# Performance work log

Hardware: AMD Instinct MI355X
Metric: run time of the kernel (lower is better)

The kernel has to match this reference:

```python
import jax, jax.numpy as jnp
import numpy as np

B, D, H, W, C = 2, 8, 56, 56, 128
NH = 4
HD = C // NH
WS = (7, 7)
HIDDEN = 4 * C
EPS = 1e-5


def layernorm(x, g, b):
    mu = jnp.mean(x, axis=-1, keepdims=True)
    var = jnp.var(x, axis=-1, keepdims=True)
    return (x - mu) * jax.lax.rsqrt(var + EPS) * g + b


def rearrange3d(x, gh, gw):
    b, d, h, w, c = x.shape
    x = x.reshape(b, d, h // gh, gh, w, c).swapaxes(2, 3).reshape(b, d, h, w, c)
    x = x.reshape(b, d, h, w // gw, gw, c).swapaxes(3, 4).reshape(b, d, h, w, c)
    return x


def restore3d(x, gh, gw):
    b, d, h, w, c = x.shape
    x = x.reshape(b, d, h, gw, w // gw, c).swapaxes(3, 4).reshape(b, d, h, w, c)
    x = x.reshape(b, d, gh, h // gh, w, c).swapaxes(2, 3).reshape(b, d, h, w, c)
    return x


def setup_inputs() -> dict:
    key = jax.random.key(0)
    ks = jax.random.split(key, 10)
    s = 0.02
    return {
        "x": jax.random.normal(ks[0], (B, D, H, W, C), jnp.float32),
        "norm1_g": jnp.ones((C,), jnp.float32),
        "norm1_b": jnp.zeros((C,), jnp.float32),
        "qkv_w": jax.random.normal(ks[1], (3 * C, C), jnp.float32) * s,
        "qkv_b": jnp.zeros((3 * C,), jnp.float32),
        "proj_w": jax.random.normal(ks[2], (C, C), jnp.float32) * s,
        "proj_b": jnp.zeros((C,), jnp.float32),
        "dw_w": jax.random.normal(ks[3], (3, 3, 1, C), jnp.float32) * s,  # HWIO depthwise
        "dw_b": jnp.zeros((C,), jnp.float32),
        "norm2_g": jnp.ones((C,), jnp.float32),
        "norm2_b": jnp.zeros((C,), jnp.float32),
        "fc1_w": jax.random.normal(ks[4], (HIDDEN, C), jnp.float32) * s,
        "fc1_b": jnp.zeros((HIDDEN,), jnp.float32),
        "fc2_w": jax.random.normal(ks[5], (C, HIDDEN), jnp.float32) * s,
        "fc2_b": jnp.zeros((C,), jnp.float32),
    }


def reference(x, norm1_g, norm1_b, qkv_w, qkv_b, proj_w, proj_b, dw_w, dw_b,
              norm2_g, norm2_b, fc1_w, fc1_b, fc2_w, fc2_b):
    b, d, h, w, c = x.shape
    gh, gw = h // WS[0], w // WS[1]  # 8, 8 (H,W divisible by window size -> no pad)
    shortcut = x

    # ---- part1: norm1 -> dwconv branch + windowed attention ----
    xn = layernorm(x, norm1_g, norm1_b)

    # depthwise 3x3 conv on each frame (B*D, H, W, C), SAME padding
    xc = jax.lax.conv_general_dilated(
        xn.reshape(b * d, h, w, c), dw_w, (1, 1), 'SAME',
        dimension_numbers=('NHWC', 'HWIO', 'NHWC'), feature_group_count=c)
    x_conv3d = (xc + dw_b).reshape(b, d, h, w, c)

    # interleaved regrouping, then window partition: (B*nW, N=D*7*7, C)
    xr = rearrange3d(xn, gh, gw)
    xw = xr.reshape(b, d, gh, WS[0], gw, WS[1], c)
    xw = xw.transpose(0, 2, 4, 1, 3, 5, 6).reshape(-1, d * WS[0] * WS[1], c)
    B_, N, _ = xw.shape

    # attention
    qkv = jnp.einsum('bnc,oc->bno', xw, qkv_w) + qkv_b
    qkv = qkv.reshape(B_, N, 3, NH, HD).transpose(2, 0, 3, 1, 4)  # (3, B_, nh, N, hd)
    q, k, v = qkv[0], qkv[1], qkv[2]
    scale = HD ** -0.5
    attn = jnp.einsum('bhnd,bhmd->bhnm', q * scale, k)
    attn = jax.nn.softmax(attn, axis=-1)
    out = jnp.einsum('bhnm,bhmd->bhnd', attn, v)
    out = out.transpose(0, 2, 1, 3).reshape(B_, N, c)
    out = jnp.einsum('bnc,oc->bno', out, proj_w) + proj_b

    # window reverse + restore grouping
    xo = out.reshape(b, gh, gw, d, WS[0], WS[1], c)
    xo = xo.transpose(0, 3, 1, 4, 2, 5, 6).reshape(b, d, h, w, c)
    xo = restore3d(xo, gh, gw)
    xo = xo + x_conv3d

    # ---- residuals + MLP ----
    x1 = shortcut + xo
    xm = layernorm(x1, norm2_g, norm2_b)
    xm = jnp.einsum('bdhwc,oc->bdhwo', xm, fc1_w) + fc1_b
    xm = jax.nn.gelu(xm, approximate=False)
    xm = jnp.einsum('bdhwo,co->bdhwc', xm, fc2_w) + fc2_b
    return x1 + xm


if __name__ == '__main__':
    inp = setup_inputs()
    y = reference(**inp)
    print(y.shape, y.dtype)
```

## Files before the change

kernel.cpp:

```cpp
#include <hip/hip_runtime.h>
#include <hip/hip_bf16.h>

#define NB 2
#define ND 8
#define NHH 56
#define NWW 56
#define NC 128
#define NHEAD 4
#define DHEAD 32
#define NSEQ 392
#define NWIN 128
#define NTOK (NB*ND*NHH*NWW)
#define NHID 512
#define EPSV 1e-5f
#define PIECE 12544

typedef unsigned int uint32;
typedef __attribute__((ext_vector_type(8))) short bf16x8;
typedef __attribute__((ext_vector_type(4))) float f32x4;
typedef __attribute__((ext_vector_type(16))) float f32x16;

__device__ __forceinline__ short f2bf(float x) {
  __hip_bfloat16 h = __float2bfloat16(x);
  return *reinterpret_cast<short*>(&h);
}
__device__ __forceinline__ float bflo(uint32 u) { return __uint_as_float(u << 16); }
__device__ __forceinline__ float bfhi(uint32 u) { return __uint_as_float(u & 0xffff0000u); }
__device__ __forceinline__ float fexp2(float x) {
  float e; asm("v_exp_f32 %0, %1" : "=v"(e) : "v"(x)); return e;
}

__device__ __forceinline__ int win_to_src(int grow) {
  int win = grow / NSEQ, n = grow % NSEQ;
  int b = win >> 6, gh = (win >> 3) & 7, gw = win & 7;
  int d = n / 49, rem = n % 49;
  int p = rem / 7, q = rem % 7;
  int h = p * 8 + gh, w = q * 8 + gw;
  return ((b * ND + d) * NHH + h) * NWW + w;
}

#define GLDS(gp, lp) \
  __builtin_amdgcn_global_load_lds( \
      (const __attribute__((address_space(1))) void*)(gp), \
      (__attribute__((address_space(3))) void*)(lp), 16, 0, 0)

__global__ void k_convw(const float* __restrict__ qkvw, const float* __restrict__ projw,
                        const float* __restrict__ fc1w, const float* __restrict__ fc2w,
                        short* __restrict__ out) {
  int i = blockIdx.x * 256 + threadIdx.x;
  float v; int n, k, K, base;
  if (i < 49152)       { v = qkvw[i];          n = i >> 7;          k = i & 127;   K = 128; base = 0; }
  else if (i < 65536)  { int l = i - 49152;  v = projw[l]; n = l >> 7; k = l & 127; K = 128; base = 49152; }
  else if (i < 131072) { int l = i - 65536;  v = fc1w[l];  n = l >> 7; k = l & 127; K = 128; base = 65536; }
  else                 { int l = i - 131072; v = fc2w[l];  n = l >> 9; k = l & 511; K = 512; base = 131072; }
  int k2 = (((k >> 3) ^ (n & 7)) << 3) | (k & 7);
  out[base + n * K + k2] = f2bf(v);
}

__global__ __launch_bounds__(256) void k_ln1(const float* __restrict__ xin,
    const float* __restrict__ g, const float* __restrict__ bsh, short* __restrict__ out) {
  int w = threadIdx.x >> 6, lane = threadIdx.x & 63;
  float g0 = g[2 * lane], g1 = g[2 * lane + 1];
  float b0 = bsh[2 * lane], b1 = bsh[2 * lane + 1];
  for (int r = blockIdx.x * 4 + w; r < NTOK; r += gridDim.x * 4) {
    int src = win_to_src(r);
    float2 v = *(const float2*)(xin + (long)src * NC + lane * 2);
    float s = v.x + v.y, s2 = v.x * v.x + v.y * v.y;
    #pragma unroll
    for (int m = 1; m < 64; m <<= 1) { s += __shfl_xor(s, m); s2 += __shfl_xor(s2, m); }
    float mu = s * (1.f / NC);
    float var = s2 * (1.f / NC) - mu * mu;
    float rr = rsqrtf(var + EPSV);
    uint32 p0 = (unsigned short)f2bf((v.x - mu) * rr * g0 + b0);
    uint32 p1 = (unsigned short)f2bf((v.y - mu) * rr * g1 + b1);
    int pos = (((lane >> 2) ^ (r & 7)) << 4) + ((lane & 3) << 2);
    *(uint32*)((char*)out + (long)r * 256 + pos) = p0 | (p1 << 16);
  }
}

__global__ void k_dwconv(const short* __restrict__ xn, const float* __restrict__ xorig,
                         const float* __restrict__ wgt, const float* __restrict__ bias,
                         short* __restrict__ out) {
  int idx = blockIdx.x * 256 + threadIdx.x;
  int cp = idx & 63;
  int wr = idx >> 6;
  int win = wr / NSEQ, n = wr % NSEQ;
  int b = win >> 6, gh = (win >> 3) & 7, gw = win & 7;
  int d = n / 49, rem = n % 49;
  int p = rem / 7, q = rem % 7;
  int h = p * 8 + gh, w = q * 8 + gw;
  int bd = b * ND + d;
  float a0 = bias[2 * cp], a1 = bias[2 * cp + 1];
  #pragma unroll
  for (int kh = 0; kh < 3; kh++) {
    int hh = h + kh - 1;
    if (hh < 0 || hh >= NHH) continue;
    #pragma unroll
    for (int kw = 0; kw < 3; kw++) {
      int ww = w + kw - 1;
      if (ww < 0 || ww >= NWW) continue;
      int wr2 = ((b << 6) + ((hh & 7) << 3) + (ww & 7)) * NSEQ
              + d * 49 + (hh >> 3) * 7 + (ww >> 3);
      int bo = (((cp >> 2) ^ (wr2 & 7)) << 4) + ((cp & 3) << 2);
      uint32 u = *(const uint32*)((const char*)xn + (long)wr2 * 256 + bo);
      a0 += bflo(u) * wgt[(kh * 3 + kw) * NC + 2 * cp];
      a1 += bfhi(u) * wgt[(kh * 3 + kw) * NC + 2 * cp + 1];
    }
  }
  int src = (bd * NHH + h) * NWW + w;
  float2 xo = *(const float2*)(xorig + ((long)src << 7) + 2 * cp);
  uint32 pk = (uint32)(unsigned short)f2bf(a0 + xo.x)
            | ((uint32)(unsigned short)f2bf(a1 + xo.y) << 16);
  *(uint32*)(out + ((long)wr << 7) + 2 * cp) = pk;
}

template <int BM, int NDIM, int KDIM, int MODE>
__global__ __launch_bounds__(256) void k_gemm_mfma(
    const short* __restrict__ A, const short* __restrict__ Wb,
    const float* __restrict__ bias, const short* __restrict__ xsum16,
    const float* __restrict__ g2, const float* __restrict__ b2,
    short* __restrict__ h0, short* __restrict__ h1,
    short* __restrict__ h2p, short* __restrict__ h3,
    void* __restrict__ O0, void* __restrict__ O1, void* __restrict__ O2) {
  constexpr int ABYTES = BM * 128;
  constexpr int MI = BM / 32;
  __shared__ char S[ABYTES + 16384];
  __shared__ int asrc[BM];
  int tid = threadIdx.x;
  int m0 = blockIdx.x * BM;
  int n0 = blockIdx.y * 128;
  int lane = tid & 63, w = tid >> 6;
  int wm = w & 1, wn = w >> 1;
  int c16 = lane & 15, g = lane >> 4;

  if constexpr (MODE == 3) {
    if (tid < BM) asrc[tid] = win_to_src(m0 + tid);
  }
  const short* Abase = A;
  int arow0 = m0;
  if constexpr (MODE == 3) {
    int pc = m0 / PIECE;
    Abase = (pc == 0) ? h0 : (pc == 1) ? h1 : (pc == 2) ? h2p : h3;
    arow0 = m0 - pc * PIECE;
  }

  f32x4 acc[MI][4];
  #pragma unroll
  for (int i = 0; i < MI; i++)
    #pragma unroll
    for (int j = 0; j < 4; j++) acc[i][j] = f32x4{0.f, 0.f, 0.f, 0.f};

  const int KSTEPS = KDIM / 64;
  for (int ks = 0; ks < KSTEPS; ks++) {
    int k0 = ks * 64;
    if (ks > 0) __syncthreads();
    #pragma unroll
    for (int i = 0; i < BM / 32; i++) {
      int idx = tid + i * 256;
      int row = idx >> 3, colq = idx & 7;
      GLDS(Abase + (long)(arow0 + row) * KDIM + k0 + colq * 8, S + (idx << 4));
    }
    #pragma unroll
    for (int i = 0; i < 4; i++) {
      int idx = tid + i * 256;
      int row = idx >> 3, colq = idx & 7;
      GLDS(Wb + (long)(n0 + row) * KDIM + k0 + colq * 8, S + ABYTES + (idx << 4));
    }
    asm volatile("s_waitcnt vmcnt(0)" ::: "memory");
    __syncthreads();
    #pragma unroll
    for (int kk = 0; kk < 2; kk++) {
      bf16x8 af[MI], bfr[4];
      #pragma unroll
      for (int i = 0; i < MI; i++) {
        int ra = wm * (BM / 2) + i * 16 + c16;
        int ba = (ra << 7) + ((g + kk * 4) << 4); ba ^= ((ra & 7) << 4);
        af[i] = *(const bf16x8*)(S + ba);
      }
      #pragma unroll
      for (int j = 0; j < 4; j++) {
        int rb = wn * 64 + j * 16 + c16;
        int bb = (rb << 7) + ((g + kk * 4) << 4); bb ^= ((rb & 7) << 4);
        bfr[j] = *(const bf16x8*)(S + ABYTES + bb);
      }
      #pragma unroll
      for (int i = 0; i < MI; i++)
        #pragma unroll
        for (int j = 0; j < 4; j++)
          acc[i][j] = __builtin_amdgcn_mfma_f32_16x16x32_bf16(af[i], bfr[j], acc[i][j], 0, 0, 0);
    }
  }
  __syncthreads();

  if constexpr (MODE == 0 || MODE == 1 || MODE == 2) {
    short* X1 = (short*)S;
    float qscale = (MODE == 0 && n0 == 0) ? 0.2550348658f : 1.0f;
    #pragma unroll
    for (int i = 0; i < MI; i++) {
      #pragma unroll
      for (int r = 0; r < 4; r++) {
        int row = wm * (BM / 2) + i * 16 + g * 4 + r;
        int sw7 = row & 7;
        #pragma unroll
        for (int j = 0; j < 4; j++) {
          int nl = wn * 64 + j * 16 + c16;
          float v = acc[i][j][r] + bias[n0 + nl];
          if constexpr (MODE == 2) {
            float u = v * (0.7978845608f + 0.035677408f * v * v);
            u = fmaxf(u, -15.f);
            float t = fexp2(u * -2.885390082f);
            v = 0.5f * v * (1.f + (1.f - t) / (1.f + t));
          } else {
            v *= qscale;
          }
          int ch = nl >> 3;
          int pos = (ch & 8) | ((ch & 7) ^ sw7);
          X1[(row << 7) + (pos << 3) + (nl & 7)] = f2bf(v);
        }
      }
    }
    __syncthreads();
    int cc = tid & 15;
    #pragma unroll
    for (int it8 = 0; it8 < BM / 16; it8++) {
      int row = it8 * 16 + (tid >> 4);
      int sw7 = row & 7;
      int pos = (cc & 8) | ((cc & 7) ^ sw7);
      uint4 val = *(const uint4*)(X1 + (row << 7) + (pos << 3));
      if constexpr (MODE == 0) {
        int m = m0 + row;
        int win = m / NSEQ, tok = m - win * NSEQ;
        short* OUT = (short*)((n0 == 0) ? O0 : (n0 == 128) ? O1 : O2);
        int head = cc >> 2, dim0 = (cc & 3) << 3;
        *(uint4*)(OUT + ((((long)(win * NHEAD + head)) * NSEQ + tok) << 5) + dim0) = val;
      } else if constexpr (MODE == 2) {
        int pco = m0 / PIECE;
        short* hpO = (pco == 0) ? h0 : (pco == 1) ? h1 : (pco == 2) ? h2p : h3;
        int mloc = m0 - pco * PIECE + row;
        *(uint4*)(hpO + ((long)mloc << 9) + n0 + (pos << 3)) = val;
      } else {
        long m = m0 + row;
        uint4 xs = *(const uint4*)(xsum16 + (m << 7) + (cc << 3));
        unsigned short* tv = (unsigned short*)&val;
        unsigned short* us = (unsigned short*)&xs;
        float xv[8];
        float s = 0.f, s2 = 0.f;
        #pragma unroll
        for (int e = 0; e < 8; e++) {
          xv[e] = bflo((uint32)tv[e]) + bflo((uint32)us[e]);
          s += xv[e]; s2 += xv[e] * xv[e];
        }
        #pragma unroll
        for (int mm = 1; mm < 16; mm <<= 1) { s += __shfl_xor(s, mm); s2 += __shfl_xor(s2, mm); }
        float mu = s * (1.f / NC);
        float var = s2 * (1.f / NC) - mu * mu;
        float rr2 = rsqrtf(var + EPSV);
        float4 gv0 = *(const float4*)(g2 + cc * 8);
        float4 gv1 = *(const float4*)(g2 + cc * 8 + 4);
        float4 bv0 = *(const float4*)(b2 + cc * 8);
        float4 bv1 = *(const float4*)(b2 + cc * 8 + 4);
        float gg[8] = {gv0.x, gv0.y, gv0.z, gv0.w, gv1.x, gv1.y, gv1.z, gv1.w};
        float bb[8] = {bv0.x, bv0.y, bv0.z, bv0.w, bv1.x, bv1.y, bv1.z, bv1.w};
        short xo[8], lo[8];
        #pragma unroll
        for (int e = 0; e < 8; e++) {
          xo[e] = f2bf(xv[e]);
          lo[e] = f2bf((xv[e] - mu) * rr2 * gg[e] + bb[e]);
        }
        *(uint4*)((short*)O0 + (m << 7) + (pos << 3)) = *(uint4*)xo;
        *(uint4*)((short*)O1 + (m << 7) + (pos << 3)) = *(uint4*)lo;
      }
    }
    return;
  }

  if constexpr (MODE == 3) {
    float* Xf = (float*)S;
    #pragma unroll
    for (int h2 = 0; h2 < 2; h2++) {
      if (h2 == 1) __syncthreads();
      if (wn == h2) {
        #pragma unroll
        for (int i = 0; i < MI; i++) {
          #pragma unroll
          for (int r = 0; r < 4; r++) {
            int row = wm * (BM / 2) + i * 16 + g * 4 + r;
            int sw7 = row & 7;
            #pragma unroll
            for (int j = 0; j < 4; j++) {
              int nl = j * 16 + c16;
              int cf = nl >> 2;
              int pos = (cf & 8) | ((cf & 7) ^ sw7);
              Xf[(row << 6) + (pos << 2) + (nl & 3)] = acc[i][j][r] + bias[h2 * 64 + nl];
            }
          }
        }
      }
      __syncthreads();
      int cf = tid & 15;
      #pragma unroll
      for (int it8 = 0; it8 < BM / 16; it8++) {
        int row = it8 * 16 + (tid >> 4);
        int sw7 = row & 7;
        int pos = (cf & 8) | ((cf & 7) ^ sw7);
        float4 vv = *(const float4*)(Xf + (row << 6) + (pos << 2));
        int cb = h2 * 8 + (cf >> 1);
        int bpos = (cb & 8) | ((cb & 7) ^ sw7);
        uint2 xu = *(const uint2*)((const short*)A + (((long)(m0 + row)) << 7) + (bpos << 3) + ((cf & 1) << 2));
        unsigned short* us = (unsigned short*)&xu;
        float ov[4];
        ov[0] = vv.x + bflo((uint32)us[0]);
        ov[1] = vv.y + bflo((uint32)us[1]);
        ov[2] = vv.z + bflo((uint32)us[2]);
        ov[3] = vv.w + bflo((uint32)us[3]);
        *(float4*)((float*)O0 + ((long)asrc[row] << 7) + h2 * 64 + (cf << 2)) = *(float4*)ov;
      }
    }
    return;
  }
}

__global__ __launch_bounds__(832) void k_attn_mfma(
    const short* __restrict__ Q,
    const short* __restrict__ Kk,
    const short* __restrict__ Vv,
    short* __restrict__ aout) {
  int wh = blockIdx.x, win = wh >> 2, head = wh & 3;
  __shared__ short Ks[NSEQ * 32];
  __shared__ short Vs[32 * 408];
  int tid = threadIdx.x;
  int lane = tid & 63, w = tid >> 6;
  int ql = lane & 31, h = lane >> 5;

  const uint4* Kg4 = (const uint4*)(Kk + (long)wh * NSEQ * DHEAD);
  for (int i = tid; i < 1568; i += 832) {
    int b = i * 16; b ^= ((b >> 6) & 7) << 4;
    *(uint4*)((char*)Ks + b) = Kg4[i];
  }
  const uint32* Vg = (const uint32*)(Vv + (long)wh * NSEQ * DHEAD);
  for (int i = tid; i < NSEQ * 16; i += 832) {
    int tok = i >> 4, dp = i & 15;
    uint32 u = Vg[i];
    Vs[(2 * dp) * 408 + tok] = (short)(u & 0xffff);
    Vs[(2 * dp + 1) * 408 + tok] = (short)(u >> 16);
  }
  if (tid < 128) {
    int r = tid >> 2, cq = tid & 3;
    *(uint2*)&Vs[r * 408 + 392 + cq * 4] = make_uint2(0, 0);
  }
  __syncthreads();

  int q0 = w * 32;
  int qrow = q0 + ql; if (qrow > NSEQ - 1) qrow = NSEQ - 1;
  const short* Qr = Q + ((long)wh * NSEQ + qrow) * DHEAD;
  bf16x8 qf0 = *(const bf16x8*)(Qr + h * 8);
  bf16x8 qf1 = *(const bf16x8*)(Qr + 16 + h * 8);
  f32x16 o;
  #pragma unroll
  for (int r = 0; r < 16; r++) o[r] = 0.f;
  float lrun = 0.f;

  for (int c = 0; c < 13; c++) {
    int kb = c * 32;
    int krow = kb + ql;
    int sw = (krow & 7) << 4;
    int b0 = krow * 64 + h * 16;
    bf16x8 kf0 = *(const bf16x8*)((char*)Ks + (b0 ^ sw));
    bf16x8 kf1 = *(const bf16x8*)((char*)Ks + ((b0 + 32) ^ sw));
    f32x16 st;
    #pragma unroll
    for (int r = 0; r < 16; r++) st[r] = 0.f;
    __builtin_amdgcn_s_setprio(1);
    st = __builtin_amdgcn_mfma_f32_32x32x16_bf16(kf0, qf0, st, 0, 0, 0);
    st = __builtin_amdgcn_mfma_f32_32x32x16_bf16(kf1, qf1, st, 0, 0, 0);
    __builtin_amdgcn_s_setprio(0);
    if (c == 12) {
      #pragma unroll
      for (int r = 4; r < 16; r++) st[r] = -10000.f;
    }
    float psum = 0.f;
    #pragma unroll
    for (int r = 0; r < 16; r++) { st[r] = fexp2(st[r]); psum += st[r]; }
    psum += __shfl_xor(psum, 32);
    lrun += psum;
    #pragma unroll
    for (int s = 0; s < 2; s++) {
      if (s == 1 && c == 12) break;
      uint32 z0, z1, z2, z3;
      float p0 = st[8 * s + 0], p1 = st[8 * s + 1], p2 = st[8 * s + 2], p3 = st[8 * s + 3];
      float p4 = st[8 * s + 4], p5 = st[8 * s + 5], p6 = st[8 * s + 6], p7 = st[8 * s + 7];
      asm("v_cvt_pk_bf16_f32 %0, %1, %2" : "=v"(z0) : "v"(p0), "v"(p1));
      asm("v_cvt_pk_bf16_f32 %0, %1, %2" : "=v"(z1) : "v"(p2), "v"(p3));
      asm("v_cvt_pk_bf16_f32 %0, %1, %2" : "=v"(z2) : "v"(p4), "v"(p5));
      asm("v_cvt_pk_bf16_f32 %0, %1, %2" : "=v"(z3) : "v"(p6), "v"(p7));
      asm("v_permlane32_swap_b32 %0, %1" : "+v"(z0), "+v"(z2));
      asm("v_permlane32_swap_b32 %0, %1" : "+v"(z1), "+v"(z3));
      union { uint32 u[4]; bf16x8 v; } pb;
      pb.u[0] = z0; pb.u[1] = z1; pb.u[2] = z2; pb.u[3] = z3;
      bf16x8 vf = *(const bf16x8*)&Vs[ql * 408 + kb + 16 * s + 8 * h];
      __builtin_amdgcn_s_setprio(1);
      o = __builtin_amdgcn_mfma_f32_32x32x16_bf16(vf, pb.v, o, 0, 0, 0);
      __builtin_amdgcn_s_setprio(0);
    }
  }
  if (q0 + ql < NSEQ) {
    float inv = 1.0f / lrun;
    int qq = q0 + ql;
    long rowb = ((long)win * NSEQ + qq) * 256;
    int sw7 = qq & 7;
    #pragma unroll
    for (int rr = 0; rr < 8; rr++) {
      int r = 2 * rr;
      int d = (r & 3) + 8 * (r >> 2) + 4 * h;
      float a0 = o[r] * inv, a1 = o[r + 1] * inv;
      uint32 pk;
      asm("v_cvt_pk_bf16_f32 %0, %1, %2" : "=v"(pk) : "v"(a0), "v"(a1));
      int ch = head * 32 + d;
      int bo = (((ch >> 3) ^ sw7) << 4) + ((ch & 7) << 1);
      *(uint32*)((char*)aout + rowb + bo) = pk;
    }
  }
}

extern "C" void kernel_launch(void* const* d_in, const int* in_sizes, int n_in,
                              void* d_out, int out_size, void* d_ws, size_t ws_size,
                              hipStream_t stream) {
  const float* x    = (const float*)d_in[0];
  const float* n1g  = (const float*)d_in[1];
  const float* n1b  = (const float*)d_in[2];
  const float* qkvw = (const float*)d_in[3];
  const float* qkvb = (const float*)d_in[4];
  const float* projw= (const float*)d_in[5];
  const float* projb= (const float*)d_in[6];
  const float* dww  = (const float*)d_in[7];
  const float* dwb  = (const float*)d_in[8];
  const float* n2g  = (const float*)d_in[9];
  const float* n2b  = (const float*)d_in[10];
  const float* fc1w = (const float*)d_in[11];
  const float* fc1b = (const float*)d_in[12];
  const float* fc2w = (const float*)d_in[13];
  const float* fc2b = (const float*)d_in[14];

  char* ws = (char*)d_ws;
  short* wb_q = (short*)(ws + 0);
  short* wb_p = wb_q + 49152;
  short* wb_1 = wb_p + 16384;
  short* wb_2 = wb_1 + 65536;
  short* xnb  = (short*)(ws + 393216);
  short* xs16 = (short*)(ws + 13238272);
  short* Qb   = (short*)(ws + 38928384);
  short* Kb   = (short*)(ws + 51773440);
  short* Vb   = (short*)(ws + 64618496);
  short* aoutb = xnb;
  short* x1b   = Qb;
  short* xmb   = Vb;
  short* hid0  = xnb;
  short* hid1  = (short*)(ws + 13238272);
  short* hid2  = (short*)(ws + 26083328);
  short* hid3  = Kb;

  k_convw<<<768, 256, 0, stream>>>(qkvw, projw, fc1w, fc2w, wb_q);
  k_ln1<<<1024, 256, 0, stream>>>(x, n1g, n1b, xnb);
  k_dwconv<<<(NTOK * 64) / 256, 256, 0, stream>>>(xnb, x, dww, dwb, xs16);
  k_gemm_mfma<128, 384, 128, 0><<<dim3(392, 3), 256, 0, stream>>>(
      xnb, wb_q, qkvb, nullptr, nullptr, nullptr,
      nullptr, nullptr, nullptr, nullptr, Qb, Kb, Vb);
  k_attn_mfma<<<NWIN * NHEAD, 832, 0, stream>>>(Qb, Kb, Vb, aoutb);
  k_gemm_mfma<64, 128, 128, 1><<<dim3(784, 1), 256, 0, stream>>>(
      aoutb, wb_p, projb, xs16, n2g, n2b,
      nullptr, nullptr, nullptr, nullptr, x1b, xmb, nullptr);
  k_gemm_mfma<128, 512, 128, 2><<<dim3(392, 4), 256, 0, stream>>>(
      xmb, wb_1, fc1b, nullptr, nullptr, nullptr,
      hid0, hid1, hid2, hid3, nullptr, nullptr, nullptr);
  k_gemm_mfma<64, 128, 512, 3><<<dim3(784, 1), 256, 0, stream>>>(
      x1b, wb_2, fc2b, nullptr, nullptr, nullptr,
      hid0, hid1, hid2, hid3, d_out, nullptr, nullptr);
}
```

Measured before the change: 152.0 us.

## Merge weight-convert and LN1 launches, shrink GEMM tiles, double-buffer fc2 GEMM

Merges the weight conversion and the first layernorm into a single launch, removing one kernel launch. Moves the fc2 GEMM into a dedicated kernel that double-buffers its LDS tiles, so the next K-step's global-to-LDS loads overlap the current MFMA work. Reduces the QKV and fc1 GEMM row tiles from 128 to 64, doubling the grid size for better CU occupancy. Each tile then reuses the loaded weights less, and the fc2 kernel uses more LDS per block.

```diff
diff --git a/kernel.cpp b/kernel.cpp
--- a/kernel.cpp
+++ b/kernel.cpp
@@ -44,25 +44,27 @@
       (const __attribute__((address_space(1))) void*)(gp), \
       (__attribute__((address_space(3))) void*)(lp), 16, 0, 0)
 
-__global__ void k_convw(const float* __restrict__ qkvw, const float* __restrict__ projw,
-                        const float* __restrict__ fc1w, const float* __restrict__ fc2w,
-                        short* __restrict__ out) {
-  int i = blockIdx.x * 256 + threadIdx.x;
-  float v; int n, k, K, base;
-  if (i < 49152)       { v = qkvw[i];          n = i >> 7;          k = i & 127;   K = 128; base = 0; }
-  else if (i < 65536)  { int l = i - 49152;  v = projw[l]; n = l >> 7; k = l & 127; K = 128; base = 49152; }
-  else if (i < 131072) { int l = i - 65536;  v = fc1w[l];  n = l >> 7; k = l & 127; K = 128; base = 65536; }
-  else                 { int l = i - 131072; v = fc2w[l];  n = l >> 9; k = l & 511; K = 512; base = 131072; }
-  int k2 = (((k >> 3) ^ (n & 7)) << 3) | (k & 7);
-  out[base + n * K + k2] = f2bf(v);
-}
-
-__global__ __launch_bounds__(256) void k_ln1(const float* __restrict__ xin,
-    const float* __restrict__ g, const float* __restrict__ bsh, short* __restrict__ out) {
+__global__ __launch_bounds__(256) void k_prep(
+    const float* __restrict__ qkvw, const float* __restrict__ projw,
+    const float* __restrict__ fc1w, const float* __restrict__ fc2w,
+    short* __restrict__ wout,
+    const float* __restrict__ xin, const float* __restrict__ g,
+    const float* __restrict__ bsh, short* __restrict__ xout) {
+  if (blockIdx.x < 768) {
+    int i = blockIdx.x * 256 + threadIdx.x;
+    float v; int n, k, K, base;
+    if (i < 49152)       { v = qkvw[i];          n = i >> 7;          k = i & 127;   K = 128; base = 0; }
+    else if (i < 65536)  { int l = i - 49152;  v = projw[l]; n = l >> 7; k = l & 127; K = 128; base = 49152; }
+    else if (i < 131072) { int l = i - 65536;  v = fc1w[l];  n = l >> 7; k = l & 127; K = 128; base = 65536; }
+    else                 { int l = i - 131072; v = fc2w[l];  n = l >> 9; k = l & 511; K = 512; base = 131072; }
+    int k2 = (((k >> 3) ^ (n & 7)) << 3) | (k & 7);
+    wout[base + n * K + k2] = f2bf(v);
+    return;
+  }
   int w = threadIdx.x >> 6, lane = threadIdx.x & 63;
   float g0 = g[2 * lane], g1 = g[2 * lane + 1];
   float b0 = bsh[2 * lane], b1 = bsh[2 * lane + 1];
-  for (int r = blockIdx.x * 4 + w; r < NTOK; r += gridDim.x * 4) {
+  for (int r = (blockIdx.x - 768) * 4 + w; r < NTOK; r += 4096) {
     int src = win_to_src(r);
     float2 v = *(const float2*)(xin + (long)src * NC + lane * 2);
     float s = v.x + v.y, s2 = v.x * v.x + v.y * v.y;
@@ -74,7 +76,7 @@
     uint32 p0 = (unsigned short)f2bf((v.x - mu) * rr * g0 + b0);
     uint32 p1 = (unsigned short)f2bf((v.y - mu) * rr * g1 + b1);
     int pos = (((lane >> 2) ^ (r & 7)) << 4) + ((lane & 3) << 2);
-    *(uint32*)((char*)out + (long)r * 256 + pos) = p0 | (p1 << 16);
+    *(uint32*)((char*)xout + (long)r * 256 + pos) = p0 | (p1 << 16);
   }
 }
 
@@ -125,7 +127,6 @@
   constexpr int ABYTES = BM * 128;
   constexpr int MI = BM / 32;
   __shared__ char S[ABYTES + 16384];
-  __shared__ int asrc[BM];
   int tid = threadIdx.x;
   int m0 = blockIdx.x * BM;
   int n0 = blockIdx.y * 128;
@@ -133,17 +134,6 @@
   int wm = w & 1, wn = w >> 1;
   int c16 = lane & 15, g = lane >> 4;
 
-  if constexpr (MODE == 3) {
-    if (tid < BM) asrc[tid] = win_to_src(m0 + tid);
-  }
-  const short* Abase = A;
-  int arow0 = m0;
-  if constexpr (MODE == 3) {
-    int pc = m0 / PIECE;
-    Abase = (pc == 0) ? h0 : (pc == 1) ? h1 : (pc == 2) ? h2p : h3;
-    arow0 = m0 - pc * PIECE;
-  }
-
   f32x4 acc[MI][4];
   #pragma unroll
   for (int i = 0; i < MI; i++)
@@ -158,7 +148,7 @@
     for (int i = 0; i < BM / 32; i++) {
       int idx = tid + i * 256;
       int row = idx >> 3, colq = idx & 7;
-      GLDS(Abase + (long)(arow0 + row) * KDIM + k0 + colq * 8, S + (idx << 4));
+      GLDS(A + (long)(m0 + row) * KDIM + k0 + colq * 8, S + (idx << 4));
     }
     #pragma unroll
     for (int i = 0; i < 4; i++) {
@@ -192,131 +182,202 @@
   }
   __syncthreads();
 
-  if constexpr (MODE == 0 || MODE == 1 || MODE == 2) {
-    short* X1 = (short*)S;
-    float qscale = (MODE == 0 && n0 == 0) ? 0.2550348658f : 1.0f;
-    #pragma unroll
-    for (int i = 0; i < MI; i++) {
-      #pragma unroll
-      for (int r = 0; r < 4; r++) {
-        int row = wm * (BM / 2) + i * 16 + g * 4 + r;
-        int sw7 = row & 7;
+  short* X1 = (short*)S;
+  float qscale = (MODE == 0 && n0 == 0) ? 0.2550348658f : 1.0f;
+  #pragma unroll
+  for (int i = 0; i < MI; i++) {
+    #pragma unroll
+    for (int r = 0; r < 4; r++) {
+      int row = wm * (BM / 2) + i * 16 + g * 4 + r;
+      int sw7 = row & 7;
+      #pragma unroll
+      for (int j = 0; j < 4; j++) {
+        int nl = wn * 64 + j * 16 + c16;
+        float v = acc[i][j][r] + bias[n0 + nl];
+        if constexpr (MODE == 2) {
+          float u = v * (0.7978845608f + 0.035677408f * v * v);
+          u = fmaxf(u, -15.f);
+          float t = fexp2(u * -2.885390082f);
+          v = 0.5f * v * (1.f + (1.f - t) / (1.f + t));
+        } else {
+          v *= qscale;
+        }
+        int ch = nl >> 3;
+        int pos = (ch & 8) | ((ch & 7) ^ sw7);
+        X1[(row << 7) + (pos << 3) + (nl & 7)] = f2bf(v);
+      }
+    }
+  }
+  __syncthreads();
+  int cc = tid & 15;
+  #pragma unroll
+  for (int it8 = 0; it8 < BM / 16; it8++) {
+    int row = it8 * 16 + (tid >> 4);
+    int sw7 = row & 7;
+    int pos = (cc & 8) | ((cc & 7) ^ sw7);
+    uint4 val = *(const uint4*)(X1 + (row << 7) + (pos << 3));
+    if constexpr (MODE == 0) {
+      int m = m0 + row;
+      int win = m / NSEQ, tok = m - win * NSEQ;
+      short* OUT = (short*)((n0 == 0) ? O0 : (n0 == 128) ? O1 : O2);
+      int head = cc >> 2, dim0 = (cc & 3) << 3;
+      *(uint4*)(OUT + ((((long)(win * NHEAD + head)) * NSEQ + tok) << 5) + dim0) = val;
+    } else if constexpr (MODE == 2) {
+      int pco = m0 / PIECE;
+      short* hpO = (pco == 0) ? h0 : (pco == 1) ? h1 : (pco == 2) ? h2p : h3;
+      int mloc = m0 - pco * PIECE + row;
+      *(uint4*)(hpO + ((long)mloc << 9) + n0 + (pos << 3)) = val;
+    } else {
+      long m = m0 + row;
+      uint4 xs = *(const uint4*)(xsum16 + (m << 7) + (cc << 3));
+      unsigned short* tv = (unsigned short*)&val;
+      unsigned short* us = (unsigned short*)&xs;
+      float xv[8];
+      float s = 0.f, s2 = 0.f;
+      #pragma unroll
+      for (int e = 0; e < 8; e++) {
+        xv[e] = bflo((uint32)tv[e]) + bflo((uint32)us[e]);
+        s += xv[e]; s2 += xv[e] * xv[e];
+      }
+      #pragma unroll
+      for (int mm = 1; mm < 16; mm <<= 1) { s += __shfl_xor(s, mm); s2 += __shfl_xor(s2, mm); }
+      float mu = s * (1.f / NC);
+      float var = s2 * (1.f / NC) - mu * mu;
+      float rr2 = rsqrtf(var + EPSV);
+      float4 gv0 = *(const float4*)(g2 + cc * 8);
+      float4 gv1 = *(const float4*)(g2 + cc * 8 + 4);
+      float4 bv0 = *(const float4*)(b2 + cc * 8);
+      float4 bv1 = *(const float4*)(b2 + cc * 8 + 4);
+      float gg[8] = {gv0.x, gv0.y, gv0.z, gv0.w, gv1.x, gv1.y, gv1.z, gv1.w};
+      float bb[8] = {bv0.x, bv0.y, bv0.z, bv0.w, bv1.x, bv1.y, bv1.z, bv1.w};
+      short xo[8], lo[8];
+      #pragma unroll
+      for (int e = 0; e < 8; e++) {
+        xo[e] = f2bf(xv[e]);
+        lo[e] = f2bf((xv[e] - mu) * rr2 * gg[e] + bb[e]);
+      }
+      *(uint4*)((short*)O0 + (m << 7) + (pos << 3)) = *(uint4*)xo;
+      *(uint4*)((short*)O1 + (m << 7) + (pos << 3)) = *(uint4*)lo;
+    }
+  }
+}
+
+__global__ __launch_bounds__(256) void k_fc2(
+    const short* __restrict__ x1, const short* __restrict__ w2,
+    const float* __restrict__ bias,
+    const short* __restrict__ h0, const short* __restrict__ h1,
+    const short* __restrict__ h2p, const short* __restrict__ h3,
+    float* __restrict__ out) {
+  __shared__ char S[2][24576];
+  __shared__ int asrc[64];
+  int tid = threadIdx.x;
+  int m0 = blockIdx.x * 64;
+  int lane = tid & 63, w = tid >> 6;
+  int wm = w & 1, wn = w >> 1;
+  int c16 = lane & 15, g = lane >> 4;
+  if (tid < 64) asrc[tid] = win_to_src(m0 + tid);
+  int pc = m0 / PIECE;
+  const short* hpA = (pc == 0) ? h0 : (pc == 1) ? h1 : (pc == 2) ? h2p : h3;
+  int arow0 = m0 - pc * PIECE;
+
+  f32x4 acc[2][4];
+  #pragma unroll
+  for (int i = 0; i < 2; i++)
+    #pragma unroll
+    for (int j = 0; j < 4; j++) acc[i][j] = f32x4{0.f, 0.f, 0.f, 0.f};
+
+#define FC2_STAGE(ks, buf) do {                                               \
+    int k0_ = (ks) * 64;                                                      \
+    _Pragma("unroll")                                                         \
+    for (int i_ = 0; i_ < 2; i_++) {                                          \
+      int idx_ = tid + i_ * 256;                                              \
+      int row_ = idx_ >> 3, colq_ = idx_ & 7;                                 \
+      GLDS(hpA + (long)(arow0 + row_) * 512 + k0_ + colq_ * 8,                \
+           S[buf] + (idx_ << 4));                                             \
+    }                                                                         \
+    _Pragma("unroll")                                                         \
+    for (int i_ = 0; i_ < 4; i_++) {                                          \
+      int idx_ = tid + i_ * 256;                                              \
+      int row_ = idx_ >> 3, colq_ = idx_ & 7;                                 \
+      GLDS(w2 + (long)row_ * 512 + k0_ + colq_ * 8,                           \
+           S[buf] + 8192 + (idx_ << 4));                                      \
+    }                                                                         \
+  } while (0)
+
+  FC2_STAGE(0, 0);
+  for (int ks = 0; ks < 8; ks++) {
+    int cur = ks & 1;
+    if (ks < 7) FC2_STAGE(ks + 1, cur ^ 1);
+    if (ks < 7) asm volatile("s_waitcnt vmcnt(6)" ::: "memory");
+    else        asm volatile("s_waitcnt vmcnt(0)" ::: "memory");
+    __builtin_amdgcn_s_barrier();
+    __builtin_amdgcn_sched_barrier(0);
+    #pragma unroll
+    for (int kk = 0; kk < 2; kk++) {
+      bf16x8 af[2], bfr[4];
+      #pragma unroll
+      for (int i = 0; i < 2; i++) {
+        int ra = wm * 32 + i * 16 + c16;
+        int ba = (ra << 7) + ((g + kk * 4) << 4); ba ^= ((ra & 7) << 4);
+        af[i] = *(const bf16x8*)(S[cur] + ba);
+      }
+      #pragma unroll
+      for (int j = 0; j < 4; j++) {
+        int rb = wn * 64 + j * 16 + c16;
+        int bb = (rb << 7) + ((g + kk * 4) << 4); bb ^= ((rb & 7) << 4);
+        bfr[j] = *(const bf16x8*)(S[cur] + 8192 + bb);
+      }
+      #pragma unroll
+      for (int i = 0; i < 2; i++)
         #pragma unroll
-        for (int j = 0; j < 4; j++) {
-          int nl = wn * 64 + j * 16 + c16;
-          float v = acc[i][j][r] + bias[n0 + nl];
-          if constexpr (MODE == 2) {
-            float u = v * (0.7978845608f + 0.035677408f * v * v);
-            u = fmaxf(u, -15.f);
-            float t = fexp2(u * -2.885390082f);
-            v = 0.5f * v * (1.f + (1.f - t) / (1.f + t));
-          } else {
-            v *= qscale;
+        for (int j = 0; j < 4; j++)
+          acc[i][j] = __builtin_amdgcn_mfma_f32_16x16x32_bf16(af[i], bfr[j], acc[i][j], 0, 0, 0);
+    }
+    __builtin_amdgcn_s_barrier();
+    __builtin_amdgcn_sched_barrier(0);
+  }
+#undef FC2_STAGE
+
+  float* Xf = (float*)S[0];
+  #pragma unroll
+  for (int h2 = 0; h2 < 2; h2++) {
+    if (h2 == 1) __syncthreads();
+    if (wn == h2) {
+      #pragma unroll
+      for (int i = 0; i < 2; i++) {
+        #pragma unroll
+        for (int r = 0; r < 4; r++) {
+          int row = wm * 32 + i * 16 + g * 4 + r;
+          int sw7 = row & 7;
+          #pragma unroll
+          for (int j = 0; j < 4; j++) {
+            int nl = j * 16 + c16;
+            int cf = nl >> 2;
+            int pos = (cf & 8) | ((cf & 7) ^ sw7);
+            Xf[(row << 6) + (pos << 2) + (nl & 3)] = acc[i][j][r] + bias[h2 * 64 + nl];
           }
-          int ch = nl >> 3;
-          int pos = (ch & 8) | ((ch & 7) ^ sw7);
-          X1[(row << 7) + (pos << 3) + (nl & 7)] = f2bf(v);
         }
       }
     }
     __syncthreads();
-    int cc = tid & 15;
-    #pragma unroll
-    for (int it8 = 0; it8 < BM / 16; it8++) {
+    int cf = tid & 15;
+    #pragma unroll
+    for (int it8 = 0; it8 < 4; it8++) {
       int row = it8 * 16 + (tid >> 4);
       int sw7 = row & 7;
-      int pos = (cc & 8) | ((cc & 7) ^ sw7);
-      uint4 val = *(const uint4*)(X1 + (row << 7) + (pos << 3));
-      if constexpr (MODE == 0) {
-        int m = m0 + row;
-        int win = m / NSEQ, tok = m - win * NSEQ;
-        short* OUT = (short*)((n0 == 0) ? O0 : (n0 == 128) ? O1 : O2);
-        int head = cc >> 2, dim0 = (cc & 3) << 3;
-        *(uint4*)(OUT + ((((long)(win * NHEAD + head)) * NSEQ + tok) << 5) + dim0) = val;
-      } else if constexpr (MODE == 2) {
-        int pco = m0 / PIECE;
-        short* hpO = (pco == 0) ? h0 : (pco == 1) ? h1 : (pco == 2) ? h2p : h3;
-        int mloc = m0 - pco * PIECE + row;
-        *(uint4*)(hpO + ((long)mloc << 9) + n0 + (pos << 3)) = val;
-      } else {
-        long m = m0 + row;
-        uint4 xs = *(const uint4*)(xsum16 + (m << 7) + (cc << 3));
-        unsigned short* tv = (unsigned short*)&val;
-        unsigned short* us = (unsigned short*)&xs;
-        float xv[8];
-        float s = 0.f, s2 = 0.f;
-        #pragma unroll
-        for (int e = 0; e < 8; e++) {
-          xv[e] = bflo((uint32)tv[e]) + bflo((uint32)us[e]);
-          s += xv[e]; s2 += xv[e] * xv[e];
-        }
-        #pragma unroll
-        for (int mm = 1; mm < 16; mm <<= 1) { s += __shfl_xor(s, mm); s2 += __shfl_xor(s2, mm); }
-        float mu = s * (1.f / NC);
-        float var = s2 * (1.f / NC) - mu * mu;
-        float rr2 = rsqrtf(var + EPSV);
-        float4 gv0 = *(const float4*)(g2 + cc * 8);
-        float4 gv1 = *(const float4*)(g2 + cc * 8 + 4);
-        float4 bv0 = *(const float4*)(b2 + cc * 8);
-        float4 bv1 = *(const float4*)(b2 + cc * 8 + 4);
-        float gg[8] = {gv0.x, gv0.y, gv0.z, gv0.w, gv1.x, gv1.y, gv1.z, gv1.w};
-        float bb[8] = {bv0.x, bv0.y, bv0.z, bv0.w, bv1.x, bv1.y, bv1.z, bv1.w};
-        short xo[8], lo[8];
-        #pragma unroll
-        for (int e = 0; e < 8; e++) {
-          xo[e] = f2bf(xv[e]);
-          lo[e] = f2bf((xv[e] - mu) * rr2 * gg[e] + bb[e]);
-        }
-        *(uint4*)((short*)O0 + (m << 7) + (pos << 3)) = *(uint4*)xo;
-        *(uint4*)((short*)O1 + (m << 7) + (pos << 3)) = *(uint4*)lo;
-      }
-    }
-    return;
-  }
-
-  if constexpr (MODE == 3) {
-    float* Xf = (float*)S;
-    #pragma unroll
-    for (int h2 = 0; h2 < 2; h2++) {
-      if (h2 == 1) __syncthreads();
-      if (wn == h2) {
-        #pragma unroll
-        for (int i = 0; i < MI; i++) {
-          #pragma unroll
-          for (int r = 0; r < 4; r++) {
-            int row = wm * (BM / 2) + i * 16 + g * 4 + r;
-            int sw7 = row & 7;
-            #pragma unroll
-            for (int j = 0; j < 4; j++) {
-              int nl = j * 16 + c16;
-              int cf = nl >> 2;
-              int pos = (cf & 8) | ((cf & 7) ^ sw7);
-              Xf[(row << 6) + (pos << 2) + (nl & 3)] = acc[i][j][r] + bias[h2 * 64 + nl];
-            }
-          }
-        }
-      }
-      __syncthreads();
-      int cf = tid & 15;
-      #pragma unroll
-      for (int it8 = 0; it8 < BM / 16; it8++) {
-        int row = it8 * 16 + (tid >> 4);
-        int sw7 = row & 7;
-        int pos = (cf & 8) | ((cf & 7) ^ sw7);
-        float4 vv = *(const float4*)(Xf + (row << 6) + (pos << 2));
-        int cb = h2 * 8 + (cf >> 1);
-        int bpos = (cb & 8) | ((cb & 7) ^ sw7);
-        uint2 xu = *(const uint2*)((const short*)A + (((long)(m0 + row)) << 7) + (bpos << 3) + ((cf & 1) << 2));
-        unsigned short* us = (unsigned short*)&xu;
-        float ov[4];
-        ov[0] = vv.x + bflo((uint32)us[0]);
-        ov[1] = vv.y + bflo((uint32)us[1]);
-        ov[2] = vv.z + bflo((uint32)us[2]);
-        ov[3] = vv.w + bflo((uint32)us[3]);
-        *(float4*)((float*)O0 + ((long)asrc[row] << 7) + h2 * 64 + (cf << 2)) = *(float4*)ov;
-      }
-    }
-    return;
+      int pos = (cf & 8) | ((cf & 7) ^ sw7);
+      float4 vv = *(const float4*)(Xf + (row << 6) + (pos << 2));
+      int cb = h2 * 8 + (cf >> 1);
+      int bpos = (cb & 8) | ((cb & 7) ^ sw7);
+      uint2 xu = *(const uint2*)(x1 + (((long)(m0 + row)) << 7) + (bpos << 3) + ((cf & 1) << 2));
+      unsigned short* us = (unsigned short*)&xu;
+      float ov[4];
+      ov[0] = vv.x + bflo((uint32)us[0]);
+      ov[1] = vv.y + bflo((uint32)us[1]);
+      ov[2] = vv.z + bflo((uint32)us[2]);
+      ov[3] = vv.w + bflo((uint32)us[3]);
+      *(float4*)(out + ((long)asrc[row] << 7) + h2 * 64 + (cf << 2)) = *(float4*)ov;
+    }
   }
 }
 
@@ -459,20 +520,18 @@
   short* hid2  = (short*)(ws + 26083328);
   short* hid3  = Kb;
 
-  k_convw<<<768, 256, 0, stream>>>(qkvw, projw, fc1w, fc2w, wb_q);
-  k_ln1<<<1024, 256, 0, stream>>>(x, n1g, n1b, xnb);
+  k_prep<<<1792, 256, 0, stream>>>(qkvw, projw, fc1w, fc2w, wb_q, x, n1g, n1b, xnb);
   k_dwconv<<<(NTOK * 64) / 256, 256, 0, stream>>>(xnb, x, dww, dwb, xs16);
-  k_gemm_mfma<128, 384, 128, 0><<<dim3(392, 3), 256, 0, stream>>>(
+  k_gemm_mfma<64, 384, 128, 0><<<dim3(784, 3), 256, 0, stream>>>(
       xnb, wb_q, qkvb, nullptr, nullptr, nullptr,
       nullptr, nullptr, nullptr, nullptr, Qb, Kb, Vb);
   k_attn_mfma<<<NWIN * NHEAD, 832, 0, stream>>>(Qb, Kb, Vb, aoutb);
   k_gemm_mfma<64, 128, 128, 1><<<dim3(784, 1), 256, 0, stream>>>(
       aoutb, wb_p, projb, xs16, n2g, n2b,
       nullptr, nullptr, nullptr, nullptr, x1b, xmb, nullptr);
-  k_gemm_mfma<128, 512, 128, 2><<<dim3(392, 4), 256, 0, stream>>>(
+  k_gemm_mfma<64, 512, 128, 2><<<dim3(784, 4), 256, 0, stream>>>(
       xmb, wb_1, fc1b, nullptr, nullptr, nullptr,
       hid0, hid1, hid2, hid3, nullptr, nullptr, nullptr);
-  k_gemm_mfma<64, 128, 512, 3><<<dim3(784, 1), 256, 0, stream>>>(
-      x1b, wb_2, fc2b, nullptr, nullptr, nullptr,
-      hid0, hid1, hid2, hid3, d_out, nullptr, nullptr);
-}
+  k_fc2<<<784, 256, 0, stream>>>(
+      x1b, wb_2, fc2b, hid0, hid1, hid2, hid3, (float*)d_out);
+}
```

Measured after the change: 142.2 us. 1.07x faster.
